# Optimization experiments

Measured on AMD Instinct MI355X. Metric: run time of the kernel, lower is better.

The kernel has to match this reference:

```python
import jax, jax.numpy as jnp
import numpy as np

C = 1536          # interim_dim
D2 = 2 * C        # 3072, fc_nlb dim
LN_EPS = 1e-5


def setup_inputs() -> dict:
    key = jax.random.key(0)
    ks = jax.random.split(key, 24)
    B, L = 32, 1024
    s = 0.02
    inp = {
        "x": jax.random.normal(ks[0], (B, C), dtype=jnp.float32),
        "lfb_feats": jax.random.normal(ks[1], (B, L, C), dtype=jnp.float32),
        # 1x1 Conv1d weights act as (C_out, C_in) matmuls
        "theta_w": jax.random.normal(ks[2], (C, C), dtype=jnp.float32) * s,
        "theta_b": jnp.zeros((C,), dtype=jnp.float32),
        "phi_w": jax.random.normal(ks[3], (C, C), dtype=jnp.float32) * s,
        "phi_b": jnp.zeros((C,), dtype=jnp.float32),
        "gi_w": jax.random.normal(ks[4], (C, C), dtype=jnp.float32) * s,
        "gi_b": jnp.zeros((C,), dtype=jnp.float32),
        "ln_g": jnp.ones((C,), dtype=jnp.float32),
        "ln_b": jnp.zeros((C,), dtype=jnp.float32),
        "fc_w": jax.random.normal(ks[5], (C, C), dtype=jnp.float32) * s,
        "fc_b": jnp.zeros((C,), dtype=jnp.float32),
        "fc_nlb_w": jax.random.normal(ks[6], (D2, D2), dtype=jnp.float32) * s,
        "fc_nlb_b": jnp.zeros((D2,), dtype=jnp.float32),
        "fc1_w": jax.random.normal(ks[7], (1, 1024), dtype=jnp.float32) * s,
        "fc1_b": jnp.zeros((1,), dtype=jnp.float32),
        "fc2_w": jax.random.normal(ks[8], (1, 1024), dtype=jnp.float32) * s,
        "fc2_b": jnp.zeros((1,), dtype=jnp.float32),
        "fc3_w": jax.random.normal(ks[9], (1, 1024), dtype=jnp.float32) * s,
        "fc3_b": jnp.zeros((1,), dtype=jnp.float32),
        "fct_w": jax.random.normal(ks[10], (1, D2), dtype=jnp.float32) * s,
        "fct_b": jnp.zeros((1,), dtype=jnp.float32),
    }
    return inp


def _layernorm(x, g, b):
    mu = jnp.mean(x, axis=-1, keepdims=True)
    var = jnp.mean(jnp.square(x - mu), axis=-1, keepdims=True)
    return (x - mu) * jax.lax.rsqrt(var + LN_EPS) * g + b


def reference(x, lfb_feats, theta_w, theta_b, phi_w, phi_b, gi_w, gi_b,
              ln_g, ln_b, fc_w, fc_b, fc_nlb_w, fc_nlb_b,
              fc1_w, fc1_b, fc2_w, fc2_b, fc3_w, fc3_b, fct_w, fct_b):
    # --- _NLBlock on feats = x.unsqueeze(1): query sequence length is 1 ---
    # note: scale = 1/sqrt(1/C) = sqrt(C) (as in the original code)
    scale = jnp.sqrt(jnp.asarray(C, dtype=x.dtype))
    theta = x @ theta_w.T + theta_b                       # (B, C)
    phi = lfb_feats @ phi_w.T + phi_b                     # (B, L, C)
    gi = lfb_feats @ gi_w.T + gi_b                        # (B, L, C)
    scores = jnp.einsum('bc,blc->bl', theta, phi) * scale  # (B, L)
    attn = jax.nn.softmax(scores, axis=-1)
    o = jnp.einsum('bl,blc->bc', attn, gi)                # (B, C)
    o = jax.nn.relu(_layernorm(o, ln_g, ln_b))
    o = o @ fc_w.T + fc_b                                 # dropout -> identity (eval)
    longterm = o + x                                      # residual, (B, C)

    # --- head ---
    feats = jnp.concatenate([x, longterm], axis=1)        # (B, 2C)
    feats = jax.nn.relu(feats @ fc_nlb_w.T + fc_nlb_b)    # dropout -> identity
    f1 = feats[:, :1024]
    f2 = feats[:, 1024:2048]
    f3 = feats[:, 2048:3072]
    p1 = f1 @ fc1_w.T + fc1_b
    p2 = f2 @ fc2_w.T + fc2_b
    p3 = f3 @ fc3_w.T + fc3_b
    pt = feats @ fct_w.T + fct_b
    return jnp.concatenate([p1, p2, p3, pt], axis=1)      # (B, 4)
```

## Files before the change

### kernel.cpp

```cpp
#include <hip/hip_runtime.h>
#include <math.h>

#define B 32
#define C 1536
#define D2 3072
#define L 1024
#define KC 64
#define KQ 16
#define CH 16
#define LPW 16

__device__ inline float dot4(float4 a, float4 b) {
    return a.x * b.x + a.y * b.y + a.z * b.z + a.w * b.w;
}

__device__ inline int sw(int row, int q) {
    return row * KC + ((q ^ ((row >> 2) & 7)) << 2);
}

__global__ __launch_bounds__(256) void transpose_k(const float* __restrict__ src,
                                                   float* __restrict__ dst, int n) {
    __shared__ float tile[32][33];
    int bx = blockIdx.x * 32, by = blockIdx.y * 32;
    int tx = threadIdx.x & 31, ty0 = threadIdx.x >> 5;
    #pragma unroll
    for (int r = 0; r < 4; ++r) {
        int ty = ty0 + r * 8;
        tile[ty][tx] = src[(size_t)(by + ty) * n + bx + tx];
    }
    __syncthreads();
    #pragma unroll
    for (int r = 0; r < 4; ++r) {
        int ty = ty0 + r * 8;
        dst[(size_t)(bx + ty) * n + by + tx] = tile[tx][ty];
    }
}

__global__ __launch_bounds__(256) void gemm32t4(const float* __restrict__ A,
                                                const float* __restrict__ W,
                                                float* __restrict__ part,
                                                int N, int K, int kchunks) {
    __shared__ float xs[32 * KC];
    __shared__ float wsm[128 * KC];
    int tid = threadIdx.x;
    int j0 = blockIdx.x * 128;
    int kb = blockIdx.y;
    int tb = tid & 7;
    int tj = tid >> 3;

    float4 acc[4];
    #pragma unroll
    for (int r = 0; r < 4; ++r) acc[r] = make_float4(0.f, 0.f, 0.f, 0.f);

    for (int c = 0; c < kchunks; ++c) {
        int k0 = (kb * kchunks + c) * KC;
        __syncthreads();
        #pragma unroll
        for (int p = 0; p < 2; ++p) {
            int f = tid + 256 * p;
            int row = f >> 4, q = f & 15;
            float4 v = *(const float4*)(A + (size_t)row * K + k0 + 4 * q);
            *(float4*)(xs + sw(row, q)) = v;
        }
        #pragma unroll
        for (int p = 0; p < 8; ++p) {
            int f = tid + 256 * p;
            int row = f >> 4, q = f & 15;
            float4 v = *(const float4*)(W + (size_t)(j0 + row) * K + k0 + 4 * q);
            *(float4*)(wsm + sw(row, q)) = v;
        }
        __syncthreads();
        #pragma unroll
        for (int kq = 0; kq < KQ; ++kq) {
            float4 xq[4], wq[4];
            #pragma unroll
            for (int r = 0; r < 4; ++r) {
                xq[r] = *(const float4*)(xs + sw(4 * tb + r, kq));
                wq[r] = *(const float4*)(wsm + sw(4 * tj + r, kq));
            }
            #pragma unroll
            for (int r = 0; r < 4; ++r) {
                acc[r].x += dot4(xq[r], wq[0]);
                acc[r].y += dot4(xq[r], wq[1]);
                acc[r].z += dot4(xq[r], wq[2]);
                acc[r].w += dot4(xq[r], wq[3]);
            }
        }
    }
    #pragma unroll
    for (int r = 0; r < 4; ++r) {
        *(float4*)(part + ((size_t)kb * 32 + 4 * tb + r) * N + j0 + 4 * tj) = acc[r];
    }
}

__global__ __launch_bounds__(256) void reduce_part(const float* __restrict__ part,
                                                   const float* __restrict__ bias,
                                                   const float* __restrict__ addx,
                                                   float* __restrict__ out,
                                                   float* __restrict__ feats,
                                                   int N, int ksplit, int mode) {
    int i = blockIdx.x * 256 + threadIdx.x;
    int b = i / N, j = i % N;
    float s = 0.f;
    for (int kk = 0; kk < ksplit; ++kk) s += part[((size_t)kk * 32 + b) * N + j];
    if (bias) s += bias[j];
    if (mode == 2) {
        float xv = addx[i];
        feats[(size_t)b * D2 + j] = xv;
        feats[(size_t)b * D2 + C + j] = s + xv;
    } else if (mode == 3) {
        out[i] = fmaxf(s, 0.f);
    } else {
        out[i] = s;
    }
}

__global__ __launch_bounds__(256) void reduce_ln_relu(const float* __restrict__ part,
                                                      const float* __restrict__ bias,
                                                      const float* __restrict__ g,
                                                      const float* __restrict__ bt,
                                                      float* __restrict__ out,
                                                      int ksplit) {
    int b = blockIdx.x, tid = threadIdx.x;
    __shared__ float r1[4], r2[4];
    float lv[6];
    float s1 = 0.f, s2 = 0.f;
    #pragma unroll
    for (int t = 0; t < 6; ++t) {
        int c = tid + 256 * t;
        float acc = 0.f;
        for (int kk = 0; kk < ksplit; ++kk) acc += part[((size_t)kk * 32 + b) * C + c];
        acc += bias[c];
        lv[t] = acc; s1 += acc; s2 += acc * acc;
    }
    #pragma unroll
    for (int off = 32; off > 0; off >>= 1) {
        s1 += __shfl_xor(s1, off, 64);
        s2 += __shfl_xor(s2, off, 64);
    }
    int wave = tid >> 6, lane = tid & 63;
    if (lane == 0) { r1[wave] = s1; r2[wave] = s2; }
    __syncthreads();
    s1 = r1[0] + r1[1] + r1[2] + r1[3];
    s2 = r2[0] + r2[1] + r2[2] + r2[3];
    float mu = s1 / (float)C;
    float var = s2 / (float)C - mu * mu;
    float rstd = 1.0f / sqrtf(var + 1e-5f);
    #pragma unroll
    for (int t = 0; t < 6; ++t) {
        int c = tid + 256 * t;
        float y = (lv[t] - mu) * rstd * g[c] + bt[c];
        out[(size_t)b * C + c] = fmaxf(y, 0.f);
    }
}

__global__ __launch_bounds__(256) void flash_k(const float* __restrict__ u,
                                               const float* __restrict__ lfb,
                                               float* __restrict__ pm,
                                               float* __restrict__ ps,
                                               float* __restrict__ pv) {
    int chunk = blockIdx.x;
    int b = blockIdx.y;
    int wave = threadIdx.x >> 6;
    int lane = threadIdx.x & 63;
    int widx = chunk * 4 + wave;

    const float scale = 39.19183588453085f;

    float uu[24];
    const float* ub = u + (size_t)b * C;
    #pragma unroll
    for (int t = 0; t < 6; ++t)
        *(float4*)(uu + 4 * t) = *(const float4*)(ub + 4 * lane + 256 * t);

    float m = -INFINITY, s = 0.f;
    float vv[24];
    #pragma unroll
    for (int t = 0; t < 24; ++t) vv[t] = 0.f;

    int l0 = chunk * (L / CH) + wave;
    for (int i = 0; i < LPW; ++i) {
        int l = l0 + i * 4;
        const float* row = lfb + ((size_t)b * L + l) * C;
        float xx[24];
        #pragma unroll
        for (int t = 0; t < 6; ++t)
            *(float4*)(xx + 4 * t) = *(const float4*)(row + 4 * lane + 256 * t);
        float d = 0.f;
        #pragma unroll
        for (int t = 0; t < 24; ++t) d += xx[t] * uu[t];
        #pragma unroll
        for (int off = 32; off > 0; off >>= 1) d += __shfl_xor(d, off, 64);
        float score = d * scale;
        float mn = fmaxf(m, score);
        float alpha = __expf(m - mn);
        float p = __expf(score - mn);
        s = s * alpha + p;
        #pragma unroll
        for (int t = 0; t < 24; ++t) vv[t] = vv[t] * alpha + p * xx[t];
        m = mn;
    }

    if (lane == 0) { pm[b * 64 + widx] = m; ps[b * 64 + widx] = s; }
    float* pvb = pv + ((size_t)b * 64 + widx) * C;
    #pragma unroll
    for (int t = 0; t < 6; ++t)
        *(float4*)(pvb + 4 * lane + 256 * t) = *(const float4*)(vv + 4 * t);
}

__global__ __launch_bounds__(256) void combine_k(const float* __restrict__ pm,
                                                 const float* __restrict__ ps,
                                                 const float* __restrict__ pv,
                                                 float* __restrict__ v) {
    int cc = blockIdx.x;
    int b = blockIdx.y;
    int tid = threadIdx.x;
    __shared__ float coef[64];
    if (tid < 64) {
        float mj = pm[b * 64 + tid];
        float M = mj;
        #pragma unroll
        for (int off = 32; off > 0; off >>= 1) M = fmaxf(M, __shfl_xor(M, off, 64));
        float ej = expf(mj - M);
        float S = ps[b * 64 + tid] * ej;
        #pragma unroll
        for (int off = 32; off > 0; off >>= 1) S += __shfl_xor(S, off, 64);
        coef[tid] = ej / S;
    }
    __syncthreads();
    int c = cc * 256 + tid;
    float acc = 0.f;
    #pragma unroll 8
    for (int j = 0; j < 64; ++j)
        acc += coef[j] * pv[((size_t)b * 64 + j) * C + c];
    v[(size_t)b * C + c] = acc;
}

__global__ __launch_bounds__(256) void heads_k(const float* __restrict__ h,
                                               const float* __restrict__ w1, const float* __restrict__ b1,
                                               const float* __restrict__ w2, const float* __restrict__ b2,
                                               const float* __restrict__ w3, const float* __restrict__ b3,
                                               const float* __restrict__ wt, const float* __restrict__ bt,
                                               float* __restrict__ out) {
    int b = blockIdx.x;
    int wave = threadIdx.x >> 6, lane = threadIdx.x & 63;
    const float* hb = h + (size_t)b * D2;
    float acc = 0.f;
    if (wave < 3) {
        const float* w = (wave == 0) ? w1 : ((wave == 1) ? w2 : w3);
        const float* hh = hb + wave * 1024;
        #pragma unroll
        for (int t = 0; t < 16; ++t) acc += hh[lane + 64 * t] * w[lane + 64 * t];
    } else {
        #pragma unroll
        for (int t = 0; t < 48; ++t) acc += hb[lane + 64 * t] * wt[lane + 64 * t];
    }
    #pragma unroll
    for (int off = 32; off > 0; off >>= 1) acc += __shfl_xor(acc, off, 64);
    if (lane == 0) {
        float bias = (wave == 0) ? b1[0] : (wave == 1) ? b2[0] : (wave == 2) ? b3[0] : bt[0];
        out[b * 4 + wave] = acc + bias;
    }
}

extern "C" void kernel_launch(void* const* d_in, const int* in_sizes, int n_in,
                              void* d_out, int out_size, void* d_ws, size_t ws_size,
                              hipStream_t stream) {
    (void)in_sizes; (void)n_in; (void)out_size; (void)ws_size;
    const float* x       = (const float*)d_in[0];
    const float* lfb     = (const float*)d_in[1];
    const float* theta_w = (const float*)d_in[2];
    const float* theta_b = (const float*)d_in[3];
    const float* phi_w   = (const float*)d_in[4];
    const float* gi_w    = (const float*)d_in[6];
    const float* gi_b    = (const float*)d_in[7];
    const float* ln_g    = (const float*)d_in[8];
    const float* ln_b    = (const float*)d_in[9];
    const float* fc_w    = (const float*)d_in[10];
    const float* fc_b    = (const float*)d_in[11];
    const float* fcn_w   = (const float*)d_in[12];
    const float* fcn_b   = (const float*)d_in[13];
    const float* w1 = (const float*)d_in[14]; const float* b1 = (const float*)d_in[15];
    const float* w2 = (const float*)d_in[16]; const float* b2 = (const float*)d_in[17];
    const float* w3 = (const float*)d_in[18]; const float* b3 = (const float*)d_in[19];
    const float* wt = (const float*)d_in[20]; const float* bt = (const float*)d_in[21];
    float* out = (float*)d_out;
    float* w = (float*)d_ws;

    float* phiT  = w;
    float* part  = w + 2359296;
    float* pv    = w + 4718592;
    float* pm    = w + 7864320;
    float* ps    = w + 7866368;
    float* theta = w + 7868416;
    float* u     = w + 7917568;
    float* vbuf  = w + 7966720;
    float* oln   = w + 8015872;
    float* feats = w + 8065024;
    float* h     = w + 8163328;

    transpose_k<<<dim3(48, 48), 256, 0, stream>>>(phi_w, phiT, C);

    gemm32t4<<<dim3(12, 12), 256, 0, stream>>>(x, theta_w, part, C, C, 2);
    reduce_part<<<192, 256, 0, stream>>>(part, theta_b, nullptr, theta, nullptr, C, 12, 0);

    gemm32t4<<<dim3(12, 12), 256, 0, stream>>>(theta, phiT, part, C, C, 2);
    reduce_part<<<192, 256, 0, stream>>>(part, nullptr, nullptr, u, nullptr, C, 12, 0);

    flash_k<<<dim3(CH, B), 256, 0, stream>>>(u, lfb, pm, ps, pv);
    combine_k<<<dim3(6, B), 256, 0, stream>>>(pm, ps, pv, vbuf);

    gemm32t4<<<dim3(12, 12), 256, 0, stream>>>(vbuf, gi_w, part, C, C, 2);
    reduce_ln_relu<<<B, 256, 0, stream>>>(part, gi_b, ln_g, ln_b, oln, 12);

    gemm32t4<<<dim3(12, 12), 256, 0, stream>>>(oln, fc_w, part, C, C, 2);
    reduce_part<<<192, 256, 0, stream>>>(part, fc_b, x, nullptr, feats, C, 12, 2);

    gemm32t4<<<dim3(24, 24), 256, 0, stream>>>(feats, fcn_w, part, D2, D2, 2);
    reduce_part<<<384, 256, 0, stream>>>(part, fcn_b, nullptr, h, nullptr, D2, 24, 3);

    heads_k<<<B, 256, 0, stream>>>(h, w1, b1, w2, b2, w3, b3, wt, bt, out);
}
```

Measured before the change: 525.2 us.

## Fuse split-K reductions into consumer kernels and drop phi_w transpose

Removes the standalone reduce_part kernels by folding the split-K partial sums, bias and residual into the A-operand load of the next GEMM, into flash_k's query-vector setup, and into the final heads kernel. The phi_w transpose kernel is replaced by a GEMM variant that loads W in row-major k-by-N order and scatters it into swizzled shared memory. This cuts several launches and intermediate round trips. In exchange, each GEMM tile reloads the 12 partial slices redundantly, and the scalar shared-memory scatter stores may cause bank conflicts.

```diff
diff --git a/kernel.cpp b/kernel.cpp
--- a/kernel.cpp
+++ b/kernel.cpp
@@ -13,33 +13,26 @@
 __device__ inline float dot4(float4 a, float4 b) {
     return a.x * b.x + a.y * b.y + a.z * b.z + a.w * b.w;
 }
+__device__ inline float4 ld4(const float* p) { return *(const float4*)p; }
+__device__ inline void   st4(float* p, float4 v) { *(float4*)p = v; }
+__device__ inline float4 add4(float4 a, float4 b) {
+    return make_float4(a.x + b.x, a.y + b.y, a.z + b.z, a.w + b.w);
+}
 
 __device__ inline int sw(int row, int q) {
     return row * KC + ((q ^ ((row >> 2) & 7)) << 2);
 }
-
-__global__ __launch_bounds__(256) void transpose_k(const float* __restrict__ src,
-                                                   float* __restrict__ dst, int n) {
-    __shared__ float tile[32][33];
-    int bx = blockIdx.x * 32, by = blockIdx.y * 32;
-    int tx = threadIdx.x & 31, ty0 = threadIdx.x >> 5;
-    #pragma unroll
-    for (int r = 0; r < 4; ++r) {
-        int ty = ty0 + r * 8;
-        tile[ty][tx] = src[(size_t)(by + ty) * n + bx + tx];
-    }
-    __syncthreads();
-    #pragma unroll
-    for (int r = 0; r < 4; ++r) {
-        int ty = ty0 + r * 8;
-        dst[(size_t)(bx + ty) * n + by + tx] = tile[tx][ty];
-    }
-}
-
-__global__ __launch_bounds__(256) void gemm32t4(const float* __restrict__ A,
-                                                const float* __restrict__ W,
-                                                float* __restrict__ part,
-                                                int N, int K, int kchunks) {
+__device__ inline int swe(int row, int k) {
+    return row * KC + (((k >> 2) ^ ((row >> 2) & 7)) << 2) + (k & 3);
+}
+
+template <int AM, int BM>
+__global__ __launch_bounds__(256) void gemm_k(const float* __restrict__ Asrc,
+                                              const float* __restrict__ abias,
+                                              const float* __restrict__ xres,
+                                              const float* __restrict__ W,
+                                              float* __restrict__ part,
+                                              int N, int K, int kchunks, int nsl) {
     __shared__ float xs[32 * KC];
     __shared__ float wsm[128 * KC];
     int tid = threadIdx.x;
@@ -59,15 +52,47 @@
         for (int p = 0; p < 2; ++p) {
             int f = tid + 256 * p;
             int row = f >> 4, q = f & 15;
-            float4 v = *(const float4*)(A + (size_t)row * K + k0 + 4 * q);
-            *(float4*)(xs + sw(row, q)) = v;
+            int k = k0 + 4 * q;
+            float4 v;
+            if (AM == 0) {
+                v = ld4(Asrc + (size_t)row * K + k);
+            } else if (AM == 1) {
+                v = ld4(abias + k);
+                #pragma unroll
+                for (int s = 0; s < 12; ++s)
+                    v = add4(v, ld4(Asrc + ((size_t)s * 32 + row) * K + k));
+            } else {
+                if (k0 < C) {
+                    v = ld4(xres + (size_t)row * C + k);
+                } else {
+                    int jj = k - C;
+                    v = add4(ld4(abias + jj), ld4(xres + (size_t)row * C + jj));
+                    #pragma unroll
+                    for (int s = 0; s < 12; ++s)
+                        v = add4(v, ld4(Asrc + ((size_t)s * 32 + row) * C + jj));
+                }
+            }
+            st4(xs + sw(row, q), v);
         }
-        #pragma unroll
-        for (int p = 0; p < 8; ++p) {
-            int f = tid + 256 * p;
-            int row = f >> 4, q = f & 15;
-            float4 v = *(const float4*)(W + (size_t)(j0 + row) * K + k0 + 4 * q);
-            *(float4*)(wsm + sw(row, q)) = v;
+        if (BM == 0) {
+            #pragma unroll
+            for (int p = 0; p < 8; ++p) {
+                int f = tid + 256 * p;
+                int row = f >> 4, q = f & 15;
+                float4 v = ld4(W + (size_t)(j0 + row) * K + k0 + 4 * q);
+                st4(wsm + sw(row, q), v);
+            }
+        } else {
+            #pragma unroll
+            for (int p = 0; p < 8; ++p) {
+                int f = tid + 256 * p;
+                int kk = f >> 5, jq = f & 31;
+                float4 v = ld4(W + (size_t)(k0 + kk) * N + j0 + 4 * jq);
+                wsm[swe(4 * jq + 0, kk)] = v.x;
+                wsm[swe(4 * jq + 1, kk)] = v.y;
+                wsm[swe(4 * jq + 2, kk)] = v.z;
+                wsm[swe(4 * jq + 3, kk)] = v.w;
+            }
         }
         __syncthreads();
         #pragma unroll
@@ -75,8 +100,8 @@
             float4 xq[4], wq[4];
             #pragma unroll
             for (int r = 0; r < 4; ++r) {
-                xq[r] = *(const float4*)(xs + sw(4 * tb + r, kq));
-                wq[r] = *(const float4*)(wsm + sw(4 * tj + r, kq));
+                xq[r] = ld4(xs + sw(4 * tb + r, kq));
+                wq[r] = ld4(wsm + sw(4 * tj + r, kq));
             }
             #pragma unroll
             for (int r = 0; r < 4; ++r) {
@@ -88,31 +113,8 @@
         }
     }
     #pragma unroll
-    for (int r = 0; r < 4; ++r) {
-        *(float4*)(part + ((size_t)kb * 32 + 4 * tb + r) * N + j0 + 4 * tj) = acc[r];
-    }
-}
-
-__global__ __launch_bounds__(256) void reduce_part(const float* __restrict__ part,
-                                                   const float* __restrict__ bias,
-                                                   const float* __restrict__ addx,
-                                                   float* __restrict__ out,
-                                                   float* __restrict__ feats,
-                                                   int N, int ksplit, int mode) {
-    int i = blockIdx.x * 256 + threadIdx.x;
-    int b = i / N, j = i % N;
-    float s = 0.f;
-    for (int kk = 0; kk < ksplit; ++kk) s += part[((size_t)kk * 32 + b) * N + j];
-    if (bias) s += bias[j];
-    if (mode == 2) {
-        float xv = addx[i];
-        feats[(size_t)b * D2 + j] = xv;
-        feats[(size_t)b * D2 + C + j] = s + xv;
-    } else if (mode == 3) {
-        out[i] = fmaxf(s, 0.f);
-    } else {
-        out[i] = s;
-    }
+    for (int r = 0; r < 4; ++r)
+        st4(part + ((size_t)kb * 32 + 4 * tb + r) * N + j0 + 4 * tj, acc[r]);
 }
 
 __global__ __launch_bounds__(256) void reduce_ln_relu(const float* __restrict__ part,
@@ -154,7 +156,7 @@
     }
 }
 
-__global__ __launch_bounds__(256) void flash_k(const float* __restrict__ u,
+__global__ __launch_bounds__(256) void flash_k(const float* __restrict__ partU,
                                                const float* __restrict__ lfb,
                                                float* __restrict__ pm,
                                                float* __restrict__ ps,
@@ -163,15 +165,25 @@
     int b = blockIdx.y;
     int wave = threadIdx.x >> 6;
     int lane = threadIdx.x & 63;
+    int tid = threadIdx.x;
     int widx = chunk * 4 + wave;
 
     const float scale = 39.19183588453085f;
 
+    __shared__ float uld[C];
+    for (int c0 = tid; c0 < C; c0 += 256) {
+        float s = 0.f;
+        #pragma unroll
+        for (int ss = 0; ss < 12; ++ss)
+            s += partU[((size_t)ss * 32 + b) * C + c0];
+        uld[c0] = s;
+    }
+    __syncthreads();
+
     float uu[24];
-    const float* ub = u + (size_t)b * C;
     #pragma unroll
     for (int t = 0; t < 6; ++t)
-        *(float4*)(uu + 4 * t) = *(const float4*)(ub + 4 * lane + 256 * t);
+        *(float4*)(uu + 4 * t) = ld4(uld + 4 * lane + 256 * t);
 
     float m = -INFINITY, s = 0.f;
     float vv[24];
@@ -185,7 +197,7 @@
         float xx[24];
         #pragma unroll
         for (int t = 0; t < 6; ++t)
-            *(float4*)(xx + 4 * t) = *(const float4*)(row + 4 * lane + 256 * t);
+            *(float4*)(xx + 4 * t) = ld4(row + 4 * lane + 256 * t);
         float d = 0.f;
         #pragma unroll
         for (int t = 0; t < 24; ++t) d += xx[t] * uu[t];
@@ -205,7 +217,7 @@
     float* pvb = pv + ((size_t)b * 64 + widx) * C;
     #pragma unroll
     for (int t = 0; t < 6; ++t)
-        *(float4*)(pvb + 4 * lane + 256 * t) = *(const float4*)(vv + 4 * t);
+        st4(pvb + 4 * lane + 256 * t, *(float4*)(vv + 4 * t));
 }
 
 __global__ __launch_bounds__(256) void combine_k(const float* __restrict__ pm,
@@ -236,30 +248,48 @@
     v[(size_t)b * C + c] = acc;
 }
 
-__global__ __launch_bounds__(256) void heads_k(const float* __restrict__ h,
+__global__ __launch_bounds__(256) void final_k(const float* __restrict__ partH,
+                                               const float* __restrict__ fcn_b,
                                                const float* __restrict__ w1, const float* __restrict__ b1,
                                                const float* __restrict__ w2, const float* __restrict__ b2,
                                                const float* __restrict__ w3, const float* __restrict__ b3,
                                                const float* __restrict__ wt, const float* __restrict__ bt,
                                                float* __restrict__ out) {
     int b = blockIdx.x;
-    int wave = threadIdx.x >> 6, lane = threadIdx.x & 63;
-    const float* hb = h + (size_t)b * D2;
-    float acc = 0.f;
-    if (wave < 3) {
-        const float* w = (wave == 0) ? w1 : ((wave == 1) ? w2 : w3);
-        const float* hh = hb + wave * 1024;
-        #pragma unroll
-        for (int t = 0; t < 16; ++t) acc += hh[lane + 64 * t] * w[lane + 64 * t];
-    } else {
-        #pragma unroll
-        for (int t = 0; t < 48; ++t) acc += hb[lane + 64 * t] * wt[lane + 64 * t];
-    }
-    #pragma unroll
-    for (int off = 32; off > 0; off >>= 1) acc += __shfl_xor(acc, off, 64);
+    int tid = threadIdx.x;
+    float ph0 = 0.f, ph1 = 0.f, ph2 = 0.f, ptv = 0.f;
+    #pragma unroll
+    for (int t = 0; t < 12; ++t) {
+        int j = tid + 256 * t;
+        float s = 0.f;
+        #pragma unroll 8
+        for (int ss = 0; ss < 24; ++ss)
+            s += partH[((size_t)ss * 32 + b) * D2 + j];
+        s += fcn_b[j];
+        s = fmaxf(s, 0.f);
+        ptv += s * wt[j];
+        int jj = tid + 256 * (t & 3);
+        if (t < 4)       ph0 += s * w1[jj];
+        else if (t < 8)  ph1 += s * w2[jj];
+        else             ph2 += s * w3[jj];
+    }
+    #pragma unroll
+    for (int off = 32; off > 0; off >>= 1) {
+        ph0 += __shfl_xor(ph0, off, 64);
+        ph1 += __shfl_xor(ph1, off, 64);
+        ph2 += __shfl_xor(ph2, off, 64);
+        ptv += __shfl_xor(ptv, off, 64);
+    }
+    __shared__ float red[4][4];
+    int wave = tid >> 6, lane = tid & 63;
     if (lane == 0) {
-        float bias = (wave == 0) ? b1[0] : (wave == 1) ? b2[0] : (wave == 2) ? b3[0] : bt[0];
-        out[b * 4 + wave] = acc + bias;
+        red[wave][0] = ph0; red[wave][1] = ph1; red[wave][2] = ph2; red[wave][3] = ptv;
+    }
+    __syncthreads();
+    if (tid < 4) {
+        float v = red[0][tid] + red[1][tid] + red[2][tid] + red[3][tid];
+        float bias = (tid == 0) ? b1[0] : (tid == 1) ? b2[0] : (tid == 2) ? b3[0] : bt[0];
+        out[b * 4 + tid] = v + bias;
     }
 }
 
@@ -287,37 +317,24 @@
     float* out = (float*)d_out;
     float* w = (float*)d_ws;
 
-    float* phiT  = w;
-    float* part  = w + 2359296;
+    float* partT = w;
+    float* partU = w + 589824;
+    float* partG = w + 1179648;
+    float* partF = w + 1769472;
+    float* partH = w + 2359296;
     float* pv    = w + 4718592;
     float* pm    = w + 7864320;
     float* ps    = w + 7866368;
-    float* theta = w + 7868416;
-    float* u     = w + 7917568;
-    float* vbuf  = w + 7966720;
-    float* oln   = w + 8015872;
-    float* feats = w + 8065024;
-    float* h     = w + 8163328;
-
-    transpose_k<<<dim3(48, 48), 256, 0, stream>>>(phi_w, phiT, C);
-
-    gemm32t4<<<dim3(12, 12), 256, 0, stream>>>(x, theta_w, part, C, C, 2);
-    reduce_part<<<192, 256, 0, stream>>>(part, theta_b, nullptr, theta, nullptr, C, 12, 0);
-
-    gemm32t4<<<dim3(12, 12), 256, 0, stream>>>(theta, phiT, part, C, C, 2);
-    reduce_part<<<192, 256, 0, stream>>>(part, nullptr, nullptr, u, nullptr, C, 12, 0);
-
-    flash_k<<<dim3(CH, B), 256, 0, stream>>>(u, lfb, pm, ps, pv);
+    float* vbuf  = w + 7868416;
+    float* oln   = w + 7917568;
+
+    gemm_k<0, 0><<<dim3(12, 12), 256, 0, stream>>>(x, nullptr, nullptr, theta_w, partT, C, C, 2, 0);
+    gemm_k<1, 1><<<dim3(12, 12), 256, 0, stream>>>(partT, theta_b, nullptr, phi_w, partU, C, C, 2, 12);
+    flash_k<<<dim3(CH, B), 256, 0, stream>>>(partU, lfb, pm, ps, pv);
     combine_k<<<dim3(6, B), 256, 0, stream>>>(pm, ps, pv, vbuf);
-
-    gemm32t4<<<dim3(12, 12), 256, 0, stream>>>(vbuf, gi_w, part, C, C, 2);
-    reduce_ln_relu<<<B, 256, 0, stream>>>(part, gi_b, ln_g, ln_b, oln, 12);
-
-    gemm32t4<<<dim3(12, 12), 256, 0, stream>>>(oln, fc_w, part, C, C, 2);
-    reduce_part<<<192, 256, 0, stream>>>(part, fc_b, x, nullptr, feats, C, 12, 2);
-
-    gemm32t4<<<dim3(24, 24), 256, 0, stream>>>(feats, fcn_w, part, D2, D2, 2);
-    reduce_part<<<384, 256, 0, stream>>>(part, fcn_b, nullptr, h, nullptr, D2, 24, 3);
-
-    heads_k<<<B, 256, 0, stream>>>(h, w1, b1, w2, b2, w3, b3, wt, bt, out);
-}
+    gemm_k<0, 0><<<dim3(12, 12), 256, 0, stream>>>(vbuf, nullptr, nullptr, gi_w, partG, C, C, 2, 0);
+    reduce_ln_relu<<<B, 256, 0, stream>>>(partG, gi_b, ln_g, ln_b, oln, 12);
+    gemm_k<0, 0><<<dim3(12, 12), 256, 0, stream>>>(oln, nullptr, nullptr, fc_w, partF, C, C, 2, 0);
+    gemm_k<2, 0><<<dim3(24, 24), 256, 0, stream>>>(partF, fc_b, x, fcn_w, partH, D2, D2, 2, 12);
+    final_k<<<B, 256, 0, stream>>>(partH, fcn_b, w1, b1, w2, b2, w3, b3, wt, bt, out);
+}
```

New measurement: 544.4 us. +3.7%, slower.

## Narrow GEMM tiles, fix split-K at 12, fuse final reduce with heads

Applied to the files above, without the earlier changes.

The split-K GEMM tile shrinks from 128 to 64 output columns with a 2x4 per-thread micro-tile, doubling the grid to fill more CUs. The fc_nlb GEMM now uses 12 K-splits of 4 chunks instead of 24 of 2, halving its partial-sum traffic. Its reduction, bias and ReLU are fused into the heads kernel, which removes the h buffer and one launch. Each GEMM also gets its own partial buffer. The costs are more A-tile reloads per output and lower register reuse per thread.

```diff
diff --git a/kernel.cpp b/kernel.cpp
--- a/kernel.cpp
+++ b/kernel.cpp
@@ -6,13 +6,14 @@
 #define D2 3072
 #define L 1024
 #define KC 64
-#define KQ 16
 #define CH 16
 #define LPW 16
 
 __device__ inline float dot4(float4 a, float4 b) {
     return a.x * b.x + a.y * b.y + a.z * b.z + a.w * b.w;
 }
+__device__ inline float4 ld4(const float* p) { return *(const float4*)p; }
+__device__ inline void   st4(float* p, float4 v) { *(float4*)p = v; }
 
 __device__ inline int sw(int row, int q) {
     return row * KC + ((q ^ ((row >> 2) & 7)) << 2);
@@ -36,21 +37,20 @@
     }
 }
 
-__global__ __launch_bounds__(256) void gemm32t4(const float* __restrict__ A,
-                                                const float* __restrict__ W,
-                                                float* __restrict__ part,
-                                                int N, int K, int kchunks) {
+__global__ __launch_bounds__(256) void gemm32(const float* __restrict__ A,
+                                              const float* __restrict__ W,
+                                              float* __restrict__ part,
+                                              int N, int K, int kchunks) {
     __shared__ float xs[32 * KC];
-    __shared__ float wsm[128 * KC];
+    __shared__ float wsm[64 * KC];
     int tid = threadIdx.x;
-    int j0 = blockIdx.x * 128;
+    int j0 = blockIdx.x * 64;
     int kb = blockIdx.y;
-    int tb = tid & 7;
-    int tj = tid >> 3;
-
-    float4 acc[4];
-    #pragma unroll
-    for (int r = 0; r < 4; ++r) acc[r] = make_float4(0.f, 0.f, 0.f, 0.f);
+    int tb = tid & 15;
+    int tj = tid >> 4;
+
+    float4 acc0 = make_float4(0.f, 0.f, 0.f, 0.f);
+    float4 acc1 = make_float4(0.f, 0.f, 0.f, 0.f);
 
     for (int c = 0; c < kchunks; ++c) {
         int k0 = (kb * kchunks + c) * KC;
@@ -59,38 +59,31 @@
         for (int p = 0; p < 2; ++p) {
             int f = tid + 256 * p;
             int row = f >> 4, q = f & 15;
-            float4 v = *(const float4*)(A + (size_t)row * K + k0 + 4 * q);
-            *(float4*)(xs + sw(row, q)) = v;
+            st4(xs + sw(row, q), ld4(A + (size_t)row * K + k0 + 4 * q));
         }
         #pragma unroll
-        for (int p = 0; p < 8; ++p) {
+        for (int p = 0; p < 4; ++p) {
             int f = tid + 256 * p;
             int row = f >> 4, q = f & 15;
-            float4 v = *(const float4*)(W + (size_t)(j0 + row) * K + k0 + 4 * q);
-            *(float4*)(wsm + sw(row, q)) = v;
+            st4(wsm + sw(row, q), ld4(W + (size_t)(j0 + row) * K + k0 + 4 * q));
         }
         __syncthreads();
         #pragma unroll
-        for (int kq = 0; kq < KQ; ++kq) {
-            float4 xq[4], wq[4];
-            #pragma unroll
-            for (int r = 0; r < 4; ++r) {
-                xq[r] = *(const float4*)(xs + sw(4 * tb + r, kq));
-                wq[r] = *(const float4*)(wsm + sw(4 * tj + r, kq));
-            }
-            #pragma unroll
-            for (int r = 0; r < 4; ++r) {
-                acc[r].x += dot4(xq[r], wq[0]);
-                acc[r].y += dot4(xq[r], wq[1]);
-                acc[r].z += dot4(xq[r], wq[2]);
-                acc[r].w += dot4(xq[r], wq[3]);
-            }
+        for (int kq = 0; kq < 16; ++kq) {
+            float4 x0 = ld4(xs + sw(2 * tb, kq));
+            float4 x1 = ld4(xs + sw(2 * tb + 1, kq));
+            float4 w0 = ld4(wsm + sw(4 * tj + 0, kq));
+            float4 w1 = ld4(wsm + sw(4 * tj + 1, kq));
+            float4 w2 = ld4(wsm + sw(4 * tj + 2, kq));
+            float4 w3 = ld4(wsm + sw(4 * tj + 3, kq));
+            acc0.x += dot4(x0, w0); acc0.y += dot4(x0, w1);
+            acc0.z += dot4(x0, w2); acc0.w += dot4(x0, w3);
+            acc1.x += dot4(x1, w0); acc1.y += dot4(x1, w1);
+            acc1.z += dot4(x1, w2); acc1.w += dot4(x1, w3);
         }
     }
-    #pragma unroll
-    for (int r = 0; r < 4; ++r) {
-        *(float4*)(part + ((size_t)kb * 32 + 4 * tb + r) * N + j0 + 4 * tj) = acc[r];
-    }
+    st4(part + ((size_t)kb * 32 + 2 * tb + 0) * N + j0 + 4 * tj, acc0);
+    st4(part + ((size_t)kb * 32 + 2 * tb + 1) * N + j0 + 4 * tj, acc1);
 }
 
 __global__ __launch_bounds__(256) void reduce_part(const float* __restrict__ part,
@@ -98,18 +91,17 @@
                                                    const float* __restrict__ addx,
                                                    float* __restrict__ out,
                                                    float* __restrict__ feats,
-                                                   int N, int ksplit, int mode) {
+                                                   int N, int mode) {
     int i = blockIdx.x * 256 + threadIdx.x;
     int b = i / N, j = i % N;
     float s = 0.f;
-    for (int kk = 0; kk < ksplit; ++kk) s += part[((size_t)kk * 32 + b) * N + j];
+    #pragma unroll
+    for (int kk = 0; kk < 12; ++kk) s += part[((size_t)kk * 32 + b) * N + j];
     if (bias) s += bias[j];
     if (mode == 2) {
         float xv = addx[i];
         feats[(size_t)b * D2 + j] = xv;
         feats[(size_t)b * D2 + C + j] = s + xv;
-    } else if (mode == 3) {
-        out[i] = fmaxf(s, 0.f);
     } else {
         out[i] = s;
     }
@@ -119,8 +111,7 @@
                                                       const float* __restrict__ bias,
                                                       const float* __restrict__ g,
                                                       const float* __restrict__ bt,
-                                                      float* __restrict__ out,
-                                                      int ksplit) {
+                                                      float* __restrict__ out) {
     int b = blockIdx.x, tid = threadIdx.x;
     __shared__ float r1[4], r2[4];
     float lv[6];
@@ -129,7 +120,8 @@
     for (int t = 0; t < 6; ++t) {
         int c = tid + 256 * t;
         float acc = 0.f;
-        for (int kk = 0; kk < ksplit; ++kk) acc += part[((size_t)kk * 32 + b) * C + c];
+        #pragma unroll
+        for (int kk = 0; kk < 12; ++kk) acc += part[((size_t)kk * 32 + b) * C + c];
         acc += bias[c];
         lv[t] = acc; s1 += acc; s2 += acc * acc;
     }
@@ -171,7 +163,7 @@
     const float* ub = u + (size_t)b * C;
     #pragma unroll
     for (int t = 0; t < 6; ++t)
-        *(float4*)(uu + 4 * t) = *(const float4*)(ub + 4 * lane + 256 * t);
+        *(float4*)(uu + 4 * t) = ld4(ub + 4 * lane + 256 * t);
 
     float m = -INFINITY, s = 0.f;
     float vv[24];
@@ -185,7 +177,7 @@
         float xx[24];
         #pragma unroll
         for (int t = 0; t < 6; ++t)
-            *(float4*)(xx + 4 * t) = *(const float4*)(row + 4 * lane + 256 * t);
+            *(float4*)(xx + 4 * t) = ld4(row + 4 * lane + 256 * t);
         float d = 0.f;
         #pragma unroll
         for (int t = 0; t < 24; ++t) d += xx[t] * uu[t];
@@ -205,7 +197,7 @@
     float* pvb = pv + ((size_t)b * 64 + widx) * C;
     #pragma unroll
     for (int t = 0; t < 6; ++t)
-        *(float4*)(pvb + 4 * lane + 256 * t) = *(const float4*)(vv + 4 * t);
+        st4(pvb + 4 * lane + 256 * t, *(float4*)(vv + 4 * t));
 }
 
 __global__ __launch_bounds__(256) void combine_k(const float* __restrict__ pm,
@@ -236,30 +228,48 @@
     v[(size_t)b * C + c] = acc;
 }
 
-__global__ __launch_bounds__(256) void heads_k(const float* __restrict__ h,
+__global__ __launch_bounds__(256) void final_k(const float* __restrict__ partH,
+                                               const float* __restrict__ fcn_b,
                                                const float* __restrict__ w1, const float* __restrict__ b1,
                                                const float* __restrict__ w2, const float* __restrict__ b2,
                                                const float* __restrict__ w3, const float* __restrict__ b3,
                                                const float* __restrict__ wt, const float* __restrict__ bt,
                                                float* __restrict__ out) {
     int b = blockIdx.x;
-    int wave = threadIdx.x >> 6, lane = threadIdx.x & 63;
-    const float* hb = h + (size_t)b * D2;
-    float acc = 0.f;
-    if (wave < 3) {
-        const float* w = (wave == 0) ? w1 : ((wave == 1) ? w2 : w3);
-        const float* hh = hb + wave * 1024;
-        #pragma unroll
-        for (int t = 0; t < 16; ++t) acc += hh[lane + 64 * t] * w[lane + 64 * t];
-    } else {
-        #pragma unroll
-        for (int t = 0; t < 48; ++t) acc += hb[lane + 64 * t] * wt[lane + 64 * t];
-    }
-    #pragma unroll
-    for (int off = 32; off > 0; off >>= 1) acc += __shfl_xor(acc, off, 64);
+    int tid = threadIdx.x;
+    float ph0 = 0.f, ph1 = 0.f, ph2 = 0.f, ptv = 0.f;
+    #pragma unroll
+    for (int t = 0; t < 12; ++t) {
+        int j = tid + 256 * t;
+        float s = 0.f;
+        #pragma unroll
+        for (int ss = 0; ss < 12; ++ss)
+            s += partH[((size_t)ss * 32 + b) * D2 + j];
+        s += fcn_b[j];
+        s = fmaxf(s, 0.f);
+        ptv += s * wt[j];
+        int jj = tid + 256 * (t & 3);
+        if (t < 4)       ph0 += s * w1[jj];
+        else if (t < 8)  ph1 += s * w2[jj];
+        else             ph2 += s * w3[jj];
+    }
+    #pragma unroll
+    for (int off = 32; off > 0; off >>= 1) {
+        ph0 += __shfl_xor(ph0, off, 64);
+        ph1 += __shfl_xor(ph1, off, 64);
+        ph2 += __shfl_xor(ph2, off, 64);
+        ptv += __shfl_xor(ptv, off, 64);
+    }
+    __shared__ float red[4][4];
+    int wave = tid >> 6, lane = tid & 63;
     if (lane == 0) {
-        float bias = (wave == 0) ? b1[0] : (wave == 1) ? b2[0] : (wave == 2) ? b3[0] : bt[0];
-        out[b * 4 + wave] = acc + bias;
+        red[wave][0] = ph0; red[wave][1] = ph1; red[wave][2] = ph2; red[wave][3] = ptv;
+    }
+    __syncthreads();
+    if (tid < 4) {
+        float v = red[0][tid] + red[1][tid] + red[2][tid] + red[3][tid];
+        float bias = (tid == 0) ? b1[0] : (tid == 1) ? b2[0] : (tid == 2) ? b3[0] : bt[0];
+        out[b * 4 + tid] = v + bias;
     }
 }
 
@@ -288,36 +298,38 @@
     float* w = (float*)d_ws;
 
     float* phiT  = w;
-    float* part  = w + 2359296;
-    float* pv    = w + 4718592;
-    float* pm    = w + 7864320;
-    float* ps    = w + 7866368;
-    float* theta = w + 7868416;
-    float* u     = w + 7917568;
-    float* vbuf  = w + 7966720;
-    float* oln   = w + 8015872;
-    float* feats = w + 8065024;
-    float* h     = w + 8163328;
+    float* partT = w + 2359296;
+    float* partU = w + 2949120;
+    float* partG = w + 3538944;
+    float* partF = w + 4128768;
+    float* partH = w + 4718592;
+    float* pv    = w + 5898240;
+    float* pm    = w + 9043968;
+    float* ps    = w + 9046016;
+    float* theta = w + 9048064;
+    float* u     = w + 9097216;
+    float* vbuf  = w + 9146368;
+    float* oln   = w + 9195520;
+    float* feats = w + 9244672;
 
     transpose_k<<<dim3(48, 48), 256, 0, stream>>>(phi_w, phiT, C);
 
-    gemm32t4<<<dim3(12, 12), 256, 0, stream>>>(x, theta_w, part, C, C, 2);
-    reduce_part<<<192, 256, 0, stream>>>(part, theta_b, nullptr, theta, nullptr, C, 12, 0);
-
-    gemm32t4<<<dim3(12, 12), 256, 0, stream>>>(theta, phiT, part, C, C, 2);
-    reduce_part<<<192, 256, 0, stream>>>(part, nullptr, nullptr, u, nullptr, C, 12, 0);
+    gemm32<<<dim3(24, 12), 256, 0, stream>>>(x, theta_w, partT, C, C, 2);
+    reduce_part<<<192, 256, 0, stream>>>(partT, theta_b, nullptr, theta, nullptr, C, 0);
+
+    gemm32<<<dim3(24, 12), 256, 0, stream>>>(theta, phiT, partU, C, C, 2);
+    reduce_part<<<192, 256, 0, stream>>>(partU, nullptr, nullptr, u, nullptr, C, 0);
 
     flash_k<<<dim3(CH, B), 256, 0, stream>>>(u, lfb, pm, ps, pv);
     combine_k<<<dim3(6, B), 256, 0, stream>>>(pm, ps, pv, vbuf);
 
-    gemm32t4<<<dim3(12, 12), 256, 0, stream>>>(vbuf, gi_w, part, C, C, 2);
-    reduce_ln_relu<<<B, 256, 0, stream>>>(part, gi_b, ln_g, ln_b, oln, 12);
-
-    gemm32t4<<<dim3(12, 12), 256, 0, stream>>>(oln, fc_w, part, C, C, 2);
-    reduce_part<<<192, 256, 0, stream>>>(part, fc_b, x, nullptr, feats, C, 12, 2);
-
-    gemm32t4<<<dim3(24, 24), 256, 0, stream>>>(feats, fcn_w, part, D2, D2, 2);
-    reduce_part<<<384, 256, 0, stream>>>(part, fcn_b, nullptr, h, nullptr, D2, 24, 3);
-
-    heads_k<<<B, 256, 0, stream>>>(h, w1, b1, w2, b2, w3, b3, wt, bt, out);
-}
+    gemm32<<<dim3(24, 12), 256, 0, stream>>>(vbuf, gi_w, partG, C, C, 2);
+    reduce_ln_relu<<<B, 256, 0, stream>>>(partG, gi_b, ln_g, ln_b, oln);
+
+    gemm32<<<dim3(24, 12), 256, 0, stream>>>(oln, fc_w, partF, C, C, 2);
+    reduce_part<<<192, 256, 0, stream>>>(partF, fc_b, x, nullptr, feats, C, 2);
+
+    gemm32<<<dim3(48, 12), 256, 0, stream>>>(feats, fcn_w, partH, D2, D2, 4);
+
+    final_k<<<B, 256, 0, stream>>>(partH, fcn_b, w1, b1, w2, b2, w3, b3, wt, bt, out);
+}
```

Result: faster. 440.3 us (-16.2%).
